# Performance work log

Measured on AMD Instinct MI355X. Metric: run time of the kernel, lower is better.

Reference implementation:

```python
import jax, jax.numpy as jnp
import numpy as np

B, H, W, K = 4, 512, 512, 8
BKG_DEPTH = 100.0  # sentinel depth for empty pixels, as in the torch module


def setup_inputs() -> dict:
    key = jax.random.key(0)
    k1, k2, k3 = jax.random.split(key, 3)
    pixel_colors = jax.random.uniform(k1, (B, H, W, K, 4), dtype=jnp.float32)
    zbuf = jax.random.normal(k2, (B, H, W, K), dtype=jnp.float32)  # <0 => invalid fragment
    pixel_labels = jax.random.randint(k3, (B, H, W, K), 0, K, dtype=jnp.int32)
    background_color = jnp.ones((3,), jnp.float32)
    return {
        "pixel_colors": pixel_colors,
        "zbuf": zbuf,
        "pixel_labels": pixel_labels,
        "background_color": background_color,
    }


def _composite(pixel_colors, zbuf, labels_f, background_color):
    """Back-to-front alpha-over compositing scan across the K layer axis."""
    Bq, Hq, Wq, Kd, _ = pixel_colors.shape
    # layer axis to front, reversed so scan runs k = K-1 .. 0 (back to front)
    cols = jnp.moveaxis(pixel_colors, 3, 0)[::-1]  # [K,B,H,W,4]
    deps = jnp.moveaxis(zbuf, 3, 0)[::-1]          # [K,B,H,W]
    labs = jnp.moveaxis(labels_f, 3, 0)[::-1]      # [K,B,H,W]

    rgb0 = jnp.broadcast_to(background_color.astype(pixel_colors.dtype), (Bq, Hq, Wq, 3)) + 0.0
    a0 = jnp.zeros((Bq, Hq, Wq), pixel_colors.dtype)
    d0 = jnp.full((Bq, Hq, Wq), BKG_DEPTH, pixel_colors.dtype)
    l0 = jnp.full((Bq, Hq, Wq), float(Kd), pixel_colors.dtype)

    def step(carry, x):
        rgb, a, d, lab = carry
        c, z, l = x
        alpha = c[..., 3]
        rgb = c[..., :3] * alpha[..., None] + rgb * (1.0 - alpha[..., None])
        a = jnp.maximum(alpha, a)
        d = jnp.where(z > 0, z * alpha + d * (1.0 - alpha), d)
        lab = jnp.where(jnp.isfinite(l), jnp.where(alpha > 0.5, l, lab), lab)
        return (rgb, a, d, lab), None

    (rgb, a, d, lab), _ = jax.lax.scan(step, (rgb0, a0, d0, l0), (cols, deps, labs))
    img = jnp.concatenate([rgb, a[..., None]], axis=-1)  # [B,H,W,4]
    return img, d, lab


def _human_images(pixel_colors, labels_int, background_color):
    """For each label n in [0,K): gather the first (front-most) fragment with that label."""
    Bq, Hq, Wq, Kd, C = pixel_colors.shape
    N = Kd
    hit = labels_int[..., None] == jnp.arange(N, dtype=labels_int.dtype)  # [B,H,W,K,N]
    hit = jnp.concatenate([hit, jnp.ones((Bq, Hq, Wq, 1, N), bool)], axis=3)  # void layer always hits
    first = jnp.argmax(hit, axis=3)  # [B,H,W,N], first k where label matches, else K
    pcv = jnp.concatenate(
        [pixel_colors, jnp.zeros((Bq, Hq, Wq, 1, C), pixel_colors.dtype)], axis=3
    )  # [B,H,W,K+1,4]
    gathered = jnp.take_along_axis(pcv, first[..., None], axis=3)  # [B,H,W,N,4]
    alpha = gathered[..., 3:4]
    rgb = gathered[..., :3] * alpha + background_color * (1.0 - alpha)
    return jnp.concatenate([rgb, alpha], axis=-1)  # [B,H,W,N,4]


def reference(pixel_colors, zbuf, pixel_labels, background_color):
    Kd = pixel_colors.shape[3]
    # labels as float with NaN marking invalid fragments (zbuf < 0), as in torch forward
    labels_f = jnp.where(zbuf < 0, jnp.nan, pixel_labels.astype(pixel_colors.dtype))
    composite_image, composite_depth, lab = _composite(pixel_colors, zbuf, labels_f, background_color)
    # labels as ints with -1 marking invalid, as in raster_each_labeled_human
    labels_int = jnp.where(zbuf < 0, -1, pixel_labels.astype(jnp.int32))
    human_images = _human_images(pixel_colors, labels_int, background_color)
    lab = jnp.where(lab > Kd - 0.5, -1.0, lab)
    composite_label = jnp.round(lab).astype(jnp.int32)
    return composite_image, composite_depth, composite_label, human_images
```

## Files before the change

### kernel.cpp

```cpp
#include <hip/hip_runtime.h>


#define BKG_DEPTH 100.0f
#define KD 8

typedef float f32x4 __attribute__((ext_vector_type(4)));

#define QP_XOR1 0xB1
#define QP_XOR2 0x4E
#define ROW_SHL(n) (0x100 | (n))
#define ROW_SHR(n) (0x110 | (n))

template <int CTRL>
__device__ __forceinline__ float dppf(float x) {
    return __int_as_float(__builtin_amdgcn_update_dpp(
        0, __float_as_int(x), CTRL, 0xF, 0xF, true));
}
template <int CTRL>
__device__ __forceinline__ int dppi(int x) {
    return __builtin_amdgcn_update_dpp(0, x, CTRL, 0xF, 0xF, true);
}

__global__ __launch_bounds__(256) void alpha_comp_dpp(
    const float4* __restrict__ pc,
    const float*  __restrict__ zb,
    const int*    __restrict__ lb,
    const float*  __restrict__ bg,
    float* __restrict__ out,
    int P)
{
    const int tid = blockIdx.x * blockDim.x + threadIdx.x;
    const int pix = tid >> 3;
    const int kk  = tid & 7;
    if (pix >= P) return;

    const float bg0 = bg[0], bg1 = bg[1], bg2 = bg[2];

    const float4 c     = pc[tid];
    const float  z     = zb[tid];
    const int    lbl   = lb[tid];
    const float  alpha = c.w;
    const bool   valid = !(z < 0.0f);

    float incl = 1.0f - alpha;
    { const float u = dppf<ROW_SHR(1)>(incl); incl = (kk >= 1) ? incl * u : incl; }
    { const float u = dppf<ROW_SHR(2)>(incl); incl = (kk >= 2) ? incl * u : incl; }
    { const float u = dppf<ROW_SHR(4)>(incl); incl = (kk >= 4) ? incl * u : incl; }
    float pre = dppf<ROW_SHR(1)>(incl); pre = (kk == 0) ? 1.0f : pre;
    const float T = dppf<ROW_SHL(7)>(incl);
    const float w = alpha * pre;

    float sr = c.x * w, sg = c.y * w, sb = c.z * w, am = alpha;
    sr += dppf<QP_XOR1>(sr); sg += dppf<QP_XOR1>(sg); sb += dppf<QP_XOR1>(sb);
    am = fmaxf(am, dppf<QP_XOR1>(am));
    sr += dppf<QP_XOR2>(sr); sg += dppf<QP_XOR2>(sg); sb += dppf<QP_XOR2>(sb);
    am = fmaxf(am, dppf<QP_XOR2>(am));
    sr += dppf<ROW_SHL(4)>(sr); sg += dppf<ROW_SHL(4)>(sg); sb += dppf<ROW_SHL(4)>(sb);
    am = fmaxf(am, dppf<ROW_SHL(4)>(am));

    const float a2 = (z > 0.0f) ? alpha : 0.0f;
    float incl2 = 1.0f - a2;
    { const float u = dppf<ROW_SHR(1)>(incl2); incl2 = (kk >= 1) ? incl2 * u : incl2; }
    { const float u = dppf<ROW_SHR(2)>(incl2); incl2 = (kk >= 2) ? incl2 * u : incl2; }
    { const float u = dppf<ROW_SHR(4)>(incl2); incl2 = (kk >= 4) ? incl2 * u : incl2; }
    float pre2 = dppf<ROW_SHR(1)>(incl2); pre2 = (kk == 0) ? 1.0f : pre2;
    const float T2 = dppf<ROW_SHL(6)>(incl2);
    float sd = z * (a2 * pre2);
    sd += dppf<QP_XOR1>(sd);
    sd += dppf<QP_XOR2>(sd);
    sd += dppf<ROW_SHL(4)>(sd);
    const float outD = fmaf(BKG_DEPTH, T2, sd);

    int pw = (valid ? lbl : 0xF) << (4 * kk);
    pw |= dppi<QP_XOR1>(pw);
    pw |= dppi<QP_XOR2>(pw);
    {
        const int lo = dppi<ROW_SHL(4)>(pw);
        const int hi = dppi<ROW_SHR(4)>(pw);
        pw |= (kk & 4) ? hi : lo;
    }

    const unsigned long long bal = __ballot(valid && (alpha > 0.5f));
    const int lane = threadIdx.x & 63;
    const unsigned grpByte = (unsigned)((bal >> (lane & ~7)) & 0xFFull);
    const int jlab = grpByte ? (__ffs(grpByte) - 1) : 0;
    const float labv = grpByte ? (float)((pw >> (4 * jlab)) & 0xF) : -1.0f;

    int jm = 8;
    #pragma unroll
    for (int j = 7; j >= 0; --j)
        jm = (((pw >> (4 * j)) & 0xF) == kk) ? j : jm;
    const bool hit = (jm < 8);
    const int src = hit ? jm : 0;
    float gx = __shfl(c.x, src, 8);
    float gy = __shfl(c.y, src, 8);
    float gz = __shfl(c.z, src, 8);
    float gw = __shfl(c.w, src, 8);
    gx = hit ? gx : 0.0f;  gy = hit ? gy : 0.0f;
    gz = hit ? gz : 0.0f;  gw = hit ? gw : 0.0f;
    const float ia = 1.0f - gw;
    const f32x4 hv = { fmaf(gx, gw, bg0 * ia),
                       fmaf(gy, gw, bg1 * ia),
                       fmaf(gz, gw, bg2 * ia),
                       gw };

    __builtin_nontemporal_store(hv, &((f32x4*)(out + (size_t)6 * P))[tid]);
    if (kk == 0) {
        const f32x4 img = { fmaf(bg0, T, sr), fmaf(bg1, T, sg), fmaf(bg2, T, sb), am };
        __builtin_nontemporal_store(img, &((f32x4*)out)[pix]);
    }
    if (kk == 1) __builtin_nontemporal_store(outD, &out[(size_t)4 * P + pix]);
    if (kk == 2) __builtin_nontemporal_store(labv, &out[(size_t)5 * P + pix]);
}

extern "C" void kernel_launch(void* const* d_in, const int* in_sizes, int n_in,
                              void* d_out, int out_size, void* d_ws, size_t ws_size,
                              hipStream_t stream) {
    const float4* pc = (const float4*)d_in[0];
    const float*  zb = (const float*)d_in[1];
    const int*    lb = (const int*)d_in[2];
    const float*  bg = (const float*)d_in[3];
    float* out = (float*)d_out;

    const int P = in_sizes[1] / KD;
    const int total = P * KD;
    const int block = 256;
    const int grid = (total + block - 1) / block;
    alpha_comp_dpp<<<grid, block, 0, stream>>>(pc, zb, lb, bg, out, P);
}
```

Before: 296.5 us.

## Use persistent grid-stride loop with software-prefetched next iteration loads

Replaces the one-thread-per-fragment launch with a grid capped at 2048 blocks, where each thread loops over fragments with a grid stride. The next iteration's color, depth and label loads are issued before the current iteration's compute, so memory latency can overlap with the DPP scan work. The aim is to reduce block launch overhead and hide load latency. The cost is extra live registers and fewer resident waves, which can lower occupancy-based latency hiding for this memory-bound kernel.

```diff
diff --git a/kernel.cpp b/kernel.cpp
--- a/kernel.cpp
+++ b/kernel.cpp
@@ -21,7 +21,7 @@
     return __builtin_amdgcn_update_dpp(0, x, CTRL, 0xF, 0xF, true);
 }
 
-__global__ __launch_bounds__(256) void alpha_comp_dpp(
+__global__ __launch_bounds__(256) void alpha_comp_pipe(
     const float4* __restrict__ pc,
     const float*  __restrict__ zb,
     const int*    __restrict__ lb,
@@ -29,88 +29,103 @@
     float* __restrict__ out,
     int P)
 {
-    const int tid = blockIdx.x * blockDim.x + threadIdx.x;
-    const int pix = tid >> 3;
-    const int kk  = tid & 7;
-    if (pix >= P) return;
+    const int stride = gridDim.x * blockDim.x;
+    const int total  = P * KD;
+    int t = blockIdx.x * blockDim.x + threadIdx.x;
+    if (t >= total) return;
 
+    const int kk   = t & 7;
+    const int lane = threadIdx.x & 63;
     const float bg0 = bg[0], bg1 = bg[1], bg2 = bg[2];
 
-    const float4 c     = pc[tid];
-    const float  z     = zb[tid];
-    const int    lbl   = lb[tid];
-    const float  alpha = c.w;
-    const bool   valid = !(z < 0.0f);
+    float4 c   = pc[t];
+    float  z   = zb[t];
+    int    lbl = lb[t];
 
-    float incl = 1.0f - alpha;
-    { const float u = dppf<ROW_SHR(1)>(incl); incl = (kk >= 1) ? incl * u : incl; }
-    { const float u = dppf<ROW_SHR(2)>(incl); incl = (kk >= 2) ? incl * u : incl; }
-    { const float u = dppf<ROW_SHR(4)>(incl); incl = (kk >= 4) ? incl * u : incl; }
-    float pre = dppf<ROW_SHR(1)>(incl); pre = (kk == 0) ? 1.0f : pre;
-    const float T = dppf<ROW_SHL(7)>(incl);
-    const float w = alpha * pre;
+    while (true) {
+        const int  tn    = t + stride;
+        const bool more  = tn < total;
+        const int  tload = more ? tn : t;
+        const float4 cn   = pc[tload];
+        const float  zn   = zb[tload];
+        const int    lbln = lb[tload];
 
-    float sr = c.x * w, sg = c.y * w, sb = c.z * w, am = alpha;
-    sr += dppf<QP_XOR1>(sr); sg += dppf<QP_XOR1>(sg); sb += dppf<QP_XOR1>(sb);
-    am = fmaxf(am, dppf<QP_XOR1>(am));
-    sr += dppf<QP_XOR2>(sr); sg += dppf<QP_XOR2>(sg); sb += dppf<QP_XOR2>(sb);
-    am = fmaxf(am, dppf<QP_XOR2>(am));
-    sr += dppf<ROW_SHL(4)>(sr); sg += dppf<ROW_SHL(4)>(sg); sb += dppf<ROW_SHL(4)>(sb);
-    am = fmaxf(am, dppf<ROW_SHL(4)>(am));
+        const int   pix   = t >> 3;
+        const float alpha = c.w;
+        const bool  valid = !(z < 0.0f);
 
-    const float a2 = (z > 0.0f) ? alpha : 0.0f;
-    float incl2 = 1.0f - a2;
-    { const float u = dppf<ROW_SHR(1)>(incl2); incl2 = (kk >= 1) ? incl2 * u : incl2; }
-    { const float u = dppf<ROW_SHR(2)>(incl2); incl2 = (kk >= 2) ? incl2 * u : incl2; }
-    { const float u = dppf<ROW_SHR(4)>(incl2); incl2 = (kk >= 4) ? incl2 * u : incl2; }
-    float pre2 = dppf<ROW_SHR(1)>(incl2); pre2 = (kk == 0) ? 1.0f : pre2;
-    const float T2 = dppf<ROW_SHL(6)>(incl2);
-    float sd = z * (a2 * pre2);
-    sd += dppf<QP_XOR1>(sd);
-    sd += dppf<QP_XOR2>(sd);
-    sd += dppf<ROW_SHL(4)>(sd);
-    const float outD = fmaf(BKG_DEPTH, T2, sd);
+        float incl = 1.0f - alpha;
+        { const float u = dppf<ROW_SHR(1)>(incl); incl = (kk >= 1) ? incl * u : incl; }
+        { const float u = dppf<ROW_SHR(2)>(incl); incl = (kk >= 2) ? incl * u : incl; }
+        { const float u = dppf<ROW_SHR(4)>(incl); incl = (kk >= 4) ? incl * u : incl; }
+        float pre = dppf<ROW_SHR(1)>(incl); pre = (kk == 0) ? 1.0f : pre;
+        const float T = dppf<ROW_SHL(7)>(incl);
+        const float w = alpha * pre;
 
-    int pw = (valid ? lbl : 0xF) << (4 * kk);
-    pw |= dppi<QP_XOR1>(pw);
-    pw |= dppi<QP_XOR2>(pw);
-    {
-        const int lo = dppi<ROW_SHL(4)>(pw);
-        const int hi = dppi<ROW_SHR(4)>(pw);
-        pw |= (kk & 4) ? hi : lo;
+        float sr = c.x * w, sg = c.y * w, sb = c.z * w, am = alpha;
+        sr += dppf<QP_XOR1>(sr); sg += dppf<QP_XOR1>(sg); sb += dppf<QP_XOR1>(sb);
+        am = fmaxf(am, dppf<QP_XOR1>(am));
+        sr += dppf<QP_XOR2>(sr); sg += dppf<QP_XOR2>(sg); sb += dppf<QP_XOR2>(sb);
+        am = fmaxf(am, dppf<QP_XOR2>(am));
+        sr += dppf<ROW_SHL(4)>(sr); sg += dppf<ROW_SHL(4)>(sg); sb += dppf<ROW_SHL(4)>(sb);
+        am = fmaxf(am, dppf<ROW_SHL(4)>(am));
+
+        const float a2 = (z > 0.0f) ? alpha : 0.0f;
+        float incl2 = 1.0f - a2;
+        { const float u = dppf<ROW_SHR(1)>(incl2); incl2 = (kk >= 1) ? incl2 * u : incl2; }
+        { const float u = dppf<ROW_SHR(2)>(incl2); incl2 = (kk >= 2) ? incl2 * u : incl2; }
+        { const float u = dppf<ROW_SHR(4)>(incl2); incl2 = (kk >= 4) ? incl2 * u : incl2; }
+        float pre2 = dppf<ROW_SHR(1)>(incl2); pre2 = (kk == 0) ? 1.0f : pre2;
+        const float T2 = dppf<ROW_SHL(6)>(incl2);
+        float sd = z * (a2 * pre2);
+        sd += dppf<QP_XOR1>(sd);
+        sd += dppf<QP_XOR2>(sd);
+        sd += dppf<ROW_SHL(4)>(sd);
+        const float outD = fmaf(BKG_DEPTH, T2, sd);
+
+        int pw = (valid ? lbl : 0xF) << (4 * kk);
+        pw |= dppi<QP_XOR1>(pw);
+        pw |= dppi<QP_XOR2>(pw);
+        {
+            const int lo = dppi<ROW_SHL(4)>(pw);
+            const int hi = dppi<ROW_SHR(4)>(pw);
+            pw |= (kk & 4) ? hi : lo;
+        }
+
+        const unsigned long long bal = __ballot(valid && (alpha > 0.5f));
+        const unsigned grpByte = (unsigned)((bal >> (lane & ~7)) & 0xFFull);
+        const int jlab = grpByte ? (__ffs(grpByte) - 1) : 0;
+        const float labv = grpByte ? (float)((pw >> (4 * jlab)) & 0xF) : -1.0f;
+
+        int jm = 8;
+        #pragma unroll
+        for (int j = 7; j >= 0; --j)
+            jm = (((pw >> (4 * j)) & 0xF) == kk) ? j : jm;
+        const bool hit = (jm < 8);
+        const int src = hit ? jm : 0;
+        float gx = __shfl(c.x, src, 8);
+        float gy = __shfl(c.y, src, 8);
+        float gz = __shfl(c.z, src, 8);
+        float gw = __shfl(c.w, src, 8);
+        gx = hit ? gx : 0.0f;  gy = hit ? gy : 0.0f;
+        gz = hit ? gz : 0.0f;  gw = hit ? gw : 0.0f;
+        const float ia = 1.0f - gw;
+        const f32x4 hv = { fmaf(gx, gw, bg0 * ia),
+                           fmaf(gy, gw, bg1 * ia),
+                           fmaf(gz, gw, bg2 * ia),
+                           gw };
+
+        __builtin_nontemporal_store(hv, &((f32x4*)(out + (size_t)6 * P))[t]);
+        if (kk == 0) {
+            const f32x4 img = { fmaf(bg0, T, sr), fmaf(bg1, T, sg), fmaf(bg2, T, sb), am };
+            __builtin_nontemporal_store(img, &((f32x4*)out)[pix]);
+        }
+        if (kk == 1) __builtin_nontemporal_store(outD, &out[(size_t)4 * P + pix]);
+        if (kk == 2) __builtin_nontemporal_store(labv, &out[(size_t)5 * P + pix]);
+
+        if (!more) break;
+        t = tn; c = cn; z = zn; lbl = lbln;
     }
-
-    const unsigned long long bal = __ballot(valid && (alpha > 0.5f));
-    const int lane = threadIdx.x & 63;
-    const unsigned grpByte = (unsigned)((bal >> (lane & ~7)) & 0xFFull);
-    const int jlab = grpByte ? (__ffs(grpByte) - 1) : 0;
-    const float labv = grpByte ? (float)((pw >> (4 * jlab)) & 0xF) : -1.0f;
-
-    int jm = 8;
-    #pragma unroll
-    for (int j = 7; j >= 0; --j)
-        jm = (((pw >> (4 * j)) & 0xF) == kk) ? j : jm;
-    const bool hit = (jm < 8);
-    const int src = hit ? jm : 0;
-    float gx = __shfl(c.x, src, 8);
-    float gy = __shfl(c.y, src, 8);
-    float gz = __shfl(c.z, src, 8);
-    float gw = __shfl(c.w, src, 8);
-    gx = hit ? gx : 0.0f;  gy = hit ? gy : 0.0f;
-    gz = hit ? gz : 0.0f;  gw = hit ? gw : 0.0f;
-    const float ia = 1.0f - gw;
-    const f32x4 hv = { fmaf(gx, gw, bg0 * ia),
-                       fmaf(gy, gw, bg1 * ia),
-                       fmaf(gz, gw, bg2 * ia),
-                       gw };
-
-    __builtin_nontemporal_store(hv, &((f32x4*)(out + (size_t)6 * P))[tid]);
-    if (kk == 0) {
-        const f32x4 img = { fmaf(bg0, T, sr), fmaf(bg1, T, sg), fmaf(bg2, T, sb), am };
-        __builtin_nontemporal_store(img, &((f32x4*)out)[pix]);
-    }
-    if (kk == 1) __builtin_nontemporal_store(outD, &out[(size_t)4 * P + pix]);
-    if (kk == 2) __builtin_nontemporal_store(labv, &out[(size_t)5 * P + pix]);
 }
 
 extern "C" void kernel_launch(void* const* d_in, const int* in_sizes, int n_in,
@@ -125,6 +140,7 @@
     const int P = in_sizes[1] / KD;
     const int total = P * KD;
     const int block = 256;
-    const int grid = (total + block - 1) / block;
-    alpha_comp_dpp<<<grid, block, 0, stream>>>(pc, zb, lb, bg, out, P);
+    int grid = (total + block - 1) / block;
+    if (grid > 2048) grid = 2048;
+    alpha_comp_pipe<<<grid, block, 0, stream>>>(pc, zb, lb, bg, out, P);
 }
```

After: 312.4 us. 5.4% more time.
